# Kernel optimization log

Hardware: AMD Instinct MI355X
Metric: run time of the kernel (lower is better)

## Reference

```python
import jax, jax.numpy as jnp
import numpy as np

N = 50000
IN_DIM = 128
HID = 64
HEADS = 4
OUT_DIM = 2
NEG_SLOPE = 0.2


def setup_inputs() -> dict:
    key = jax.random.key(0)
    ks = jax.random.split(key, 10)
    x = jax.random.normal(ks[0], (N, IN_DIM), dtype=jnp.float32)
    edge_index = jax.random.randint(ks[1], (2, 800000), 0, N, dtype=jnp.int64)
    s = 0.1
    W1 = jax.random.normal(ks[2], (IN_DIM, HEADS * HID), dtype=jnp.float32) * s
    att_src1 = jax.random.normal(ks[3], (HEADS, HID), dtype=jnp.float32) * s
    att_dst1 = jax.random.normal(ks[4], (HEADS, HID), dtype=jnp.float32) * s
    b1 = jnp.zeros((HEADS * HID,), dtype=jnp.float32)
    W2 = jax.random.normal(ks[5], (HEADS * HID, 1 * OUT_DIM), dtype=jnp.float32) * s
    att_src2 = jax.random.normal(ks[6], (1, OUT_DIM), dtype=jnp.float32) * s
    att_dst2 = jax.random.normal(ks[7], (1, OUT_DIM), dtype=jnp.float32) * s
    b2 = jnp.zeros((OUT_DIM,), dtype=jnp.float32)
    return {"x": x, "edge_index": edge_index, "W1": W1, "att_src1": att_src1,
            "att_dst1": att_dst1, "b1": b1, "W2": W2, "att_src2": att_src2,
            "att_dst2": att_dst2, "b2": b2}


def gat_conv(x, W, att_src, att_dst, b, src, dst, heads, ch):
    # x: [N, F_in] -> h: [N, H, C]
    n = x.shape[0]
    h = (x @ W).reshape(n, heads, ch)
    a_s = jnp.einsum('nhc,hc->nh', h, att_src)  # [N, H]
    a_d = jnp.einsum('nhc,hc->nh', h, att_dst)  # [N, H]
    e = jax.nn.leaky_relu(a_s[src] + a_d[dst], NEG_SLOPE)  # [E, H]
    # segment softmax over incoming edges of each destination node
    m = jax.ops.segment_max(e, dst, num_segments=n)
    ex = jnp.exp(e - m[dst])
    z = jax.ops.segment_sum(ex, dst, num_segments=n)
    alpha = ex / z[dst]  # [E, H]
    msg = h[src] * alpha[:, :, None]  # [E, H, C]
    out = jax.ops.segment_sum(msg, dst, num_segments=n)  # [N, H, C]
    return out.reshape(n, heads * ch) + b


def reference(x, edge_index, W1, att_src1, att_dst1, b1, W2, att_src2, att_dst2, b2):
    n = x.shape[0]
    loop = jnp.arange(n, dtype=edge_index.dtype)
    src = jnp.concatenate([edge_index[0], loop])  # add_self_loops (PyG default)
    dst = jnp.concatenate([edge_index[1], loop])
    h = gat_conv(x, W1, att_src1, att_dst1, b1, src, dst, HEADS, HID)
    h = jax.nn.elu(h)
    # dropout is identity at inference
    out = gat_conv(h, W2, att_src2, att_dst2, b2, src, dst, 1, OUT_DIM)
    return out
```

## Files before the change

### kernel.cpp

```cpp
#include <hip/hip_runtime.h>

#define NN     50000
#define E_RAW  800000
#define ETOT   (E_RAW + NN)
#define FIN    128
#define FH     256
#define NEG    0.2f
#define BCAP   64

#define P_PART 8
#define DPW    6250
#define R_REP  32
#define EPW    (E_RAW / R_REP)
#define CNT_WGS (P_PART * R_REP)
#define PREP_WGS 8
#define SC2_NB  (P_PART * R_REP)
#define GEMM_NB ((NN + 63) / 64)

typedef __attribute__((ext_vector_type(8))) short s16x8;
typedef __attribute__((ext_vector_type(4))) float f32x4;

static __device__ __forceinline__ float leaky(float v) { return v > 0.f ? v : NEG * v; }

static __device__ __forceinline__ unsigned short f2bf(float f) {
    unsigned u = __float_as_uint(f);
    unsigned r = u + 0x7fffu + ((u >> 16) & 1u);
    return (unsigned short)(r >> 16);
}

__global__ __launch_bounds__(1024) void k_count(const int* __restrict__ ei,
                                                const float* __restrict__ W1,
                                                unsigned short* __restrict__ Wt_bf,
                                                int* __restrict__ pcnt)
{
    const int t = threadIdx.x;
    if (blockIdx.x >= CNT_WGS) {
        const int base = (blockIdx.x - CNT_WGS) * 4096;
        for (int i = t; i < 4096; i += 1024) {
            int idx = base + i;
            int k = idx >> 8, col = idx & 255;
            Wt_bf[col * FIN + k] = f2bf(W1[k * FH + col]);
        }
        return;
    }
    __shared__ int lcnt[DPW];
    const int p  = blockIdx.x >> 5;
    const int r  = blockIdx.x & 31;
    const int lo = p * DPW;
    for (int i = t; i < DPW; i += 1024) lcnt[i] = 0;
    __syncthreads();
    const int ebase = r * EPW, eend = ebase + EPW;
    for (int e0 = ebase + t * 4; e0 < eend; e0 += 4096) {
        int4 dv4 = *(const int4*)&ei[E_RAW + e0];
#pragma unroll
        for (int k = 0; k < 4; k++) {
            unsigned rel = (unsigned)((&dv4.x)[k] - lo);
            if (rel < DPW) atomicAdd(&lcnt[rel], 1);
        }
    }
    __syncthreads();
    for (int i = t; i < DPW; i += 1024)
        pcnt[r * NN + lo + i] = lcnt[i];
}

__global__ __launch_bounds__(1024) void k_gx(const float* __restrict__ x,
                                             const unsigned short* __restrict__ Wt_bf,
                                             const float* __restrict__ att_src,
                                             const float* __restrict__ att_dst,
                                             const int* __restrict__ ei,
                                             const int* __restrict__ pcnt,
                                             int* __restrict__ cnt,
                                             int* __restrict__ csr_src,
                                             unsigned short* __restrict__ h1b,
                                             float* __restrict__ a_s,
                                             float* __restrict__ a_d)
{
    __shared__ __align__(16) unsigned char SbufRaw[64 * 256 * 2];
    const int t = threadIdx.x;

    if (blockIdx.x < SC2_NB) {
        int* cur = (int*)SbufRaw;
        const int p  = blockIdx.x >> 5;
        const int r  = blockIdx.x & 31;
        const int lo = p * DPW;
        for (int i = t; i < DPW; i += 1024) {
            int d = lo + i;
            int run = 1;
            for (int rr = 0; rr < r; rr++)
                run += pcnt[rr * NN + d];
            cur[i] = run;
            if (r == R_REP - 1) cnt[d] = run + pcnt[r * NN + d];
            if (r == 0) csr_src[(size_t)d << 6] = d;
        }
        __syncthreads();
        const int ebase = r * EPW, eend = ebase + EPW;
        for (int e0 = ebase + t * 4; e0 < eend; e0 += 4096) {
            int4 sv4 = *(const int4*)&ei[e0];
            int4 dv4 = *(const int4*)&ei[E_RAW + e0];
#pragma unroll
            for (int k = 0; k < 4; k++) {
                int d = (&dv4.x)[k];
                unsigned rel = (unsigned)(d - lo);
                if (rel < DPW) {
                    int pos = atomicAdd(&cur[rel], 1);
                    if (pos < BCAP)
                        csr_src[((size_t)d << 6) + pos] = (&sv4.x)[k];
                }
            }
        }
        return;
    }

    if (t >= 256) return;
    unsigned short* Sbuf = (unsigned short*)SbufRaw;
    const int w    = t >> 6;
    const int lane = t & 63;
    const int li   = lane & 15;
    const int q8   = (lane >> 4) * 8;
    const int quad = lane >> 4;
    const int n0   = (blockIdx.x - SC2_NB) * 64;

    {
        const int node_l = t >> 2;
        const int k0 = (t & 3) * 32;
        int nn = n0 + node_l; if (nn >= NN) nn = NN - 1;
        const float* xp = &x[(size_t)nn * FIN + k0];
        unsigned short* xd = &Sbuf[node_l * 136 + k0];
#pragma unroll
        for (int i = 0; i < 8; i++) {
            float4 v = *(const float4*)&xp[i * 4];
            xd[i * 4 + 0] = f2bf(v.x);
            xd[i * 4 + 1] = f2bf(v.y);
            xd[i * 4 + 2] = f2bf(v.z);
            xd[i * 4 + 3] = f2bf(v.w);
        }
    }
    __syncthreads();

    f32x4 acc[4][4];
#pragma unroll
    for (int i = 0; i < 4; i++)
#pragma unroll
        for (int j = 0; j < 4; j++) acc[i][j] = (f32x4){0.f, 0.f, 0.f, 0.f};

#pragma unroll
    for (int kki = 0; kki < 4; kki++) {
        const int kk = kki * 32;
        s16x8 af[4], bf[4];
#pragma unroll
        for (int n16 = 0; n16 < 4; n16++) {
            int col = w * 64 + n16 * 16 + li;
            bf[n16] = *(const s16x8*)&Wt_bf[col * FIN + kk + q8];
        }
#pragma unroll
        for (int m16 = 0; m16 < 4; m16++)
            af[m16] = *(const s16x8*)&Sbuf[(m16 * 16 + li) * 136 + kk + q8];
#pragma unroll
        for (int m16 = 0; m16 < 4; m16++)
#pragma unroll
            for (int n16 = 0; n16 < 4; n16++)
                acc[m16][n16] = __builtin_amdgcn_mfma_f32_16x16x32_bf16(
                    af[m16], bf[n16], acc[m16][n16], 0, 0, 0);
    }

    {
        float as_c[4], ad_c[4];
#pragma unroll
        for (int n16 = 0; n16 < 4; n16++) {
            int col = w * 64 + n16 * 16 + li;
            as_c[n16] = att_src[col];
            ad_c[n16] = att_dst[col];
        }
#pragma unroll
        for (int m16 = 0; m16 < 4; m16++) {
            float ps[4], pd[4];
#pragma unroll
            for (int reg = 0; reg < 4; reg++) {
                float s = 0.f, d = 0.f;
#pragma unroll
                for (int n16 = 0; n16 < 4; n16++) {
                    s += acc[m16][n16][reg] * as_c[n16];
                    d += acc[m16][n16][reg] * ad_c[n16];
                }
                ps[reg] = s; pd[reg] = d;
            }
#pragma unroll
            for (int off = 1; off < 16; off <<= 1) {
#pragma unroll
                for (int reg = 0; reg < 4; reg++) {
                    ps[reg] += __shfl_xor(ps[reg], off);
                    pd[reg] += __shfl_xor(pd[reg], off);
                }
            }
            if (li == 0) {
#pragma unroll
                for (int reg = 0; reg < 4; reg++) {
                    int node = n0 + m16 * 16 + quad * 4 + reg;
                    if (node < NN) {
                        a_s[node * 4 + w] = ps[reg];
                        a_d[node * 4 + w] = pd[reg];
                    }
                }
            }
        }
    }

    __syncthreads();
#pragma unroll
    for (int m16 = 0; m16 < 4; m16++)
#pragma unroll
        for (int n16 = 0; n16 < 4; n16++)
#pragma unroll
            for (int reg = 0; reg < 4; reg++)
                Sbuf[(m16 * 16 + quad * 4 + reg) * FH + w * 64 + n16 * 16 + li] =
                    f2bf(acc[m16][n16][reg]);
    __syncthreads();
    {
        const int node_l = t >> 2;
        const int c0 = (t & 3) * 64;
        int node = n0 + node_l;
        if (node < NN) {
#pragma unroll
            for (int i = 0; i < 8; i++)
                *(uint4*)&h1b[(size_t)node * FH + c0 + i * 8] =
                    *(const uint4*)&Sbuf[node_l * FH + c0 + i * 8];
        }
    }
}

__global__ __launch_bounds__(256) void k_agg1(const int* __restrict__ cnt,
                                              const int* __restrict__ csr_src,
                                              const float* __restrict__ a_s1,
                                              const float* __restrict__ a_d1,
                                              const unsigned short* __restrict__ h1b,
                                              const float* __restrict__ b1,
                                              const float* __restrict__ W2,
                                              const float* __restrict__ att_src2,
                                              const float* __restrict__ att_dst2,
                                              float4* __restrict__ nd4)
{
    const int lane = threadIdx.x & 63;
    const int n = blockIdx.x * 4 + (threadIdx.x >> 6);
    if (n >= NN) return;
    int m = cnt[n]; if (m > BCAP) m = BCAP;
    const int h = lane >> 4;
    const float ad_h = a_d1[n * 4 + h];
    float acc0 = 0.f, acc1 = 0.f, acc2 = 0.f, acc3 = 0.f, z = 0.f;
    const int* sp = &csr_src[(size_t)n << 6];
#pragma unroll 4
    for (int j = 0; j < m; j++) {
        int s = sp[j];
        float as_h = a_s1[s * 4 + h];
        float ex = __expf(leaky(as_h + ad_h));
        unsigned long long wv =
            *(const unsigned long long*)(h1b + (size_t)s * FH + lane * 4);
        unsigned lo = (unsigned)wv, hi = (unsigned)(wv >> 32);
        acc0 += __uint_as_float(lo << 16) * ex;
        acc1 += __uint_as_float(lo & 0xffff0000u) * ex;
        acc2 += __uint_as_float(hi << 16) * ex;
        acc3 += __uint_as_float(hi & 0xffff0000u) * ex;
        z += ex;
    }
    const int c0 = lane * 4;
    float4 bb = *(const float4*)&b1[c0];
    float v0 = acc0 / z + bb.x;
    float v1 = acc1 / z + bb.y;
    float v2 = acc2 / z + bb.z;
    float v3 = acc3 / z + bb.w;
    v0 = v0 > 0.f ? v0 : __expf(v0) - 1.f;
    v1 = v1 > 0.f ? v1 : __expf(v1) - 1.f;
    v2 = v2 > 0.f ? v2 : __expf(v2) - 1.f;
    v3 = v3 > 0.f ? v3 : __expf(v3) - 1.f;
    float4 w2a = *(const float4*)&W2[c0 * 2];
    float4 w2b = *(const float4*)&W2[c0 * 2 + 4];
    float s0 = v0 * w2a.x + v1 * w2a.z + v2 * w2b.x + v3 * w2b.z;
    float s1 = v0 * w2a.y + v1 * w2a.w + v2 * w2b.y + v3 * w2b.w;
#pragma unroll
    for (int off = 32; off; off >>= 1) {
        s0 += __shfl_xor(s0, off);
        s1 += __shfl_xor(s1, off);
    }
    if (lane == 0) {
        float4 nd;
        nd.x = s0; nd.y = s1;
        nd.z = s0 * att_src2[0] + s1 * att_src2[1];
        nd.w = s0 * att_dst2[0] + s1 * att_dst2[1];
        nd4[n] = nd;
    }
}

__global__ __launch_bounds__(256) void k_agg2(const int* __restrict__ cnt,
                                              const int* __restrict__ csr_src,
                                              const float4* __restrict__ nd4,
                                              const float* __restrict__ b2,
                                              float* __restrict__ out)
{
    const int l = threadIdx.x & 15;
    const int n = blockIdx.x * 16 + (threadIdx.x >> 4);
    if (n >= NN) return;
    int m = cnt[n]; if (m > BCAP) m = BCAP;
    const int* sp = &csr_src[(size_t)n << 6];
    const float ad = nd4[n].w;
    float z = 0.f, a0 = 0.f, a1 = 0.f;
    for (int j = l; j < m; j += 16) {
        int s = sp[j];
        float4 f = nd4[s];
        float ex = __expf(leaky(f.z + ad));
        z  += ex;
        a0 += f.x * ex;
        a1 += f.y * ex;
    }
#pragma unroll
    for (int off = 8; off; off >>= 1) {
        z  += __shfl_xor(z, off);
        a0 += __shfl_xor(a0, off);
        a1 += __shfl_xor(a1, off);
    }
    if (l == 0) {
        out[n * 2 + 0] = a0 / z + b2[0];
        out[n * 2 + 1] = a1 / z + b2[1];
    }
}

extern "C" void kernel_launch(void* const* d_in, const int* in_sizes, int n_in,
                              void* d_out, int out_size, void* d_ws, size_t ws_size,
                              hipStream_t stream)
{
    const float* x        = (const float*)d_in[0];
    const int*   ei       = (const int*)d_in[1];
    const float* W1       = (const float*)d_in[2];
    const float* att_src1 = (const float*)d_in[3];
    const float* att_dst1 = (const float*)d_in[4];
    const float* b1       = (const float*)d_in[5];
    const float* W2       = (const float*)d_in[6];
    const float* att_src2 = (const float*)d_in[7];
    const float* att_dst2 = (const float*)d_in[8];
    const float* b2       = (const float*)d_in[9];
    float* out = (float*)d_out;

    int*    csr_src = (int*)d_ws;
    unsigned short* h1b = (unsigned short*)(csr_src + (size_t)NN * 64);
    unsigned short* Wt_bf = h1b + (size_t)NN * FH;
    int*    pcnt  = (int*)(Wt_bf + FH * FIN);
    int*    cnt   = pcnt + (size_t)NN * R_REP;
    float*  a_s1  = (float*)(cnt + NN);
    float*  a_d1  = a_s1 + (size_t)NN * 4;
    float4* nd4   = (float4*)(a_d1 + (size_t)NN * 4);

    k_count<<<CNT_WGS + PREP_WGS, 1024, 0, stream>>>(ei, W1, Wt_bf, pcnt);
    k_gx<<<SC2_NB + GEMM_NB, 1024, 0, stream>>>(x, Wt_bf, att_src1, att_dst1, ei,
                                                pcnt, cnt, csr_src, h1b, a_s1, a_d1);
    k_agg1<<<(NN + 3) / 4, 256, 0, stream>>>(cnt, csr_src, a_s1, a_d1, h1b,
                                             b1, W2, att_src2, att_dst2, nd4);
    k_agg2<<<(NN + 15) / 16, 256, 0, stream>>>(cnt, csr_src, nd4, b2, out);
}
```

Measured before the change: 228.3 us.

## Move GEMM into count kernel and split CSR scatter into its own launch

Restructures the front of the pipeline: a small prep kernel converts W1 to transposed bf16, then one 256-thread kernel runs both the per-partition degree counting and the layer-1 GEMM with attention logits, and a separate kernel does the CSR scatter. The GEMM no longer shares a launch with the scatter, where its 1024-thread blocks left 768 threads idle, and now overlaps with the counting pass instead. It adds an extra launch, and the front kernel still redundantly rewrites Wt_bf in its prep blocks while GEMM blocks read it, which is a benign race since the values are identical. Counting blocks drop to 256 threads, so each block processes its edge slice with fewer threads.

```diff
diff --git a/kernel.cpp b/kernel.cpp
--- a/kernel.cpp
+++ b/kernel.cpp
@@ -13,8 +13,7 @@
 #define R_REP  32
 #define EPW    (E_RAW / R_REP)
 #define CNT_WGS (P_PART * R_REP)
-#define PREP_WGS 8
-#define SC2_NB  (P_PART * R_REP)
+#define PREP_NB 8
 #define GEMM_NB ((NN + 63) / 64)
 
 typedef __attribute__((ext_vector_type(8))) short s16x8;
@@ -28,97 +27,60 @@
     return (unsigned short)(r >> 16);
 }
 
-__global__ __launch_bounds__(1024) void k_count(const int* __restrict__ ei,
-                                                const float* __restrict__ W1,
-                                                unsigned short* __restrict__ Wt_bf,
-                                                int* __restrict__ pcnt)
-{
+__global__ __launch_bounds__(256) void k_front(const int* __restrict__ ei,
+                                               const float* __restrict__ W1,
+                                               const float* __restrict__ x,
+                                               const unsigned short* __restrict__ Wt_bf_c,
+                                               unsigned short* __restrict__ Wt_bf,
+                                               int* __restrict__ pcnt,
+                                               const float* __restrict__ att_src,
+                                               const float* __restrict__ att_dst,
+                                               unsigned short* __restrict__ h1b,
+                                               float* __restrict__ a_s,
+                                               float* __restrict__ a_d)
+{
+    __shared__ __align__(16) unsigned char SbufRaw[64 * 256 * 2];
     const int t = threadIdx.x;
-    if (blockIdx.x >= CNT_WGS) {
+
+    if (blockIdx.x < CNT_WGS) {
+        int* lcnt = (int*)SbufRaw;
+        const int p  = blockIdx.x >> 5;
+        const int r  = blockIdx.x & 31;
+        const int lo = p * DPW;
+        for (int i = t; i < DPW; i += 256) lcnt[i] = 0;
+        __syncthreads();
+        const int ebase = r * EPW, eend = ebase + EPW;
+        for (int e0 = ebase + t * 4; e0 < eend; e0 += 1024) {
+            int4 dv4 = *(const int4*)&ei[E_RAW + e0];
+#pragma unroll
+            for (int k = 0; k < 4; k++) {
+                unsigned rel = (unsigned)((&dv4.x)[k] - lo);
+                if (rel < DPW) atomicAdd(&lcnt[rel], 1);
+            }
+        }
+        __syncthreads();
+        for (int i = t; i < DPW; i += 256)
+            pcnt[r * NN + lo + i] = lcnt[i];
+        return;
+    }
+
+    if (blockIdx.x < CNT_WGS + PREP_NB) {
         const int base = (blockIdx.x - CNT_WGS) * 4096;
-        for (int i = t; i < 4096; i += 1024) {
+        for (int i = t; i < 4096; i += 256) {
             int idx = base + i;
             int k = idx >> 8, col = idx & 255;
             Wt_bf[col * FIN + k] = f2bf(W1[k * FH + col]);
         }
         return;
     }
-    __shared__ int lcnt[DPW];
-    const int p  = blockIdx.x >> 5;
-    const int r  = blockIdx.x & 31;
-    const int lo = p * DPW;
-    for (int i = t; i < DPW; i += 1024) lcnt[i] = 0;
-    __syncthreads();
-    const int ebase = r * EPW, eend = ebase + EPW;
-    for (int e0 = ebase + t * 4; e0 < eend; e0 += 4096) {
-        int4 dv4 = *(const int4*)&ei[E_RAW + e0];
-#pragma unroll
-        for (int k = 0; k < 4; k++) {
-            unsigned rel = (unsigned)((&dv4.x)[k] - lo);
-            if (rel < DPW) atomicAdd(&lcnt[rel], 1);
-        }
-    }
-    __syncthreads();
-    for (int i = t; i < DPW; i += 1024)
-        pcnt[r * NN + lo + i] = lcnt[i];
-}
-
-__global__ __launch_bounds__(1024) void k_gx(const float* __restrict__ x,
-                                             const unsigned short* __restrict__ Wt_bf,
-                                             const float* __restrict__ att_src,
-                                             const float* __restrict__ att_dst,
-                                             const int* __restrict__ ei,
-                                             const int* __restrict__ pcnt,
-                                             int* __restrict__ cnt,
-                                             int* __restrict__ csr_src,
-                                             unsigned short* __restrict__ h1b,
-                                             float* __restrict__ a_s,
-                                             float* __restrict__ a_d)
-{
-    __shared__ __align__(16) unsigned char SbufRaw[64 * 256 * 2];
-    const int t = threadIdx.x;
-
-    if (blockIdx.x < SC2_NB) {
-        int* cur = (int*)SbufRaw;
-        const int p  = blockIdx.x >> 5;
-        const int r  = blockIdx.x & 31;
-        const int lo = p * DPW;
-        for (int i = t; i < DPW; i += 1024) {
-            int d = lo + i;
-            int run = 1;
-            for (int rr = 0; rr < r; rr++)
-                run += pcnt[rr * NN + d];
-            cur[i] = run;
-            if (r == R_REP - 1) cnt[d] = run + pcnt[r * NN + d];
-            if (r == 0) csr_src[(size_t)d << 6] = d;
-        }
-        __syncthreads();
-        const int ebase = r * EPW, eend = ebase + EPW;
-        for (int e0 = ebase + t * 4; e0 < eend; e0 += 4096) {
-            int4 sv4 = *(const int4*)&ei[e0];
-            int4 dv4 = *(const int4*)&ei[E_RAW + e0];
-#pragma unroll
-            for (int k = 0; k < 4; k++) {
-                int d = (&dv4.x)[k];
-                unsigned rel = (unsigned)(d - lo);
-                if (rel < DPW) {
-                    int pos = atomicAdd(&cur[rel], 1);
-                    if (pos < BCAP)
-                        csr_src[((size_t)d << 6) + pos] = (&sv4.x)[k];
-                }
-            }
-        }
-        return;
-    }
-
-    if (t >= 256) return;
+
     unsigned short* Sbuf = (unsigned short*)SbufRaw;
     const int w    = t >> 6;
     const int lane = t & 63;
     const int li   = lane & 15;
     const int q8   = (lane >> 4) * 8;
     const int quad = lane >> 4;
-    const int n0   = (blockIdx.x - SC2_NB) * 64;
+    const int n0   = (blockIdx.x - CNT_WGS - PREP_NB) * 64;
 
     {
         const int node_l = t >> 2;
@@ -150,7 +112,7 @@
 #pragma unroll
         for (int n16 = 0; n16 < 4; n16++) {
             int col = w * 64 + n16 * 16 + li;
-            bf[n16] = *(const s16x8*)&Wt_bf[col * FIN + kk + q8];
+            bf[n16] = *(const s16x8*)&Wt_bf_c[col * FIN + kk + q8];
         }
 #pragma unroll
         for (int m16 = 0; m16 < 4; m16++)
@@ -224,6 +186,43 @@
             for (int i = 0; i < 8; i++)
                 *(uint4*)&h1b[(size_t)node * FH + c0 + i * 8] =
                     *(const uint4*)&Sbuf[node_l * FH + c0 + i * 8];
+        }
+    }
+}
+
+__global__ __launch_bounds__(1024) void k_scat(const int* __restrict__ ei,
+                                               const int* __restrict__ pcnt,
+                                               int* __restrict__ cnt,
+                                               int* __restrict__ csr_src)
+{
+    __shared__ int cur[DPW];
+    const int t  = threadIdx.x;
+    const int p  = blockIdx.x >> 5;
+    const int r  = blockIdx.x & 31;
+    const int lo = p * DPW;
+    for (int i = t; i < DPW; i += 1024) {
+        int d = lo + i;
+        int run = 1;
+        for (int rr = 0; rr < r; rr++)
+            run += pcnt[rr * NN + d];
+        cur[i] = run;
+        if (r == R_REP - 1) cnt[d] = run + pcnt[r * NN + d];
+        if (r == 0) csr_src[(size_t)d << 6] = d;
+    }
+    __syncthreads();
+    const int ebase = r * EPW, eend = ebase + EPW;
+    for (int e0 = ebase + t * 4; e0 < eend; e0 += 4096) {
+        int4 sv4 = *(const int4*)&ei[e0];
+        int4 dv4 = *(const int4*)&ei[E_RAW + e0];
+#pragma unroll
+        for (int k = 0; k < 4; k++) {
+            int d = (&dv4.x)[k];
+            unsigned rel = (unsigned)(d - lo);
+            if (rel < DPW) {
+                int pos = atomicAdd(&cur[rel], 1);
+                if (pos < BCAP)
+                    csr_src[((size_t)d << 6) + pos] = (&sv4.x)[k];
+            }
         }
     }
 }
@@ -347,9 +346,24 @@
     float*  a_d1  = a_s1 + (size_t)NN * 4;
     float4* nd4   = (float4*)(a_d1 + (size_t)NN * 4);
 
-    k_count<<<CNT_WGS + PREP_WGS, 1024, 0, stream>>>(ei, W1, Wt_bf, pcnt);
-    k_gx<<<SC2_NB + GEMM_NB, 1024, 0, stream>>>(x, Wt_bf, att_src1, att_dst1, ei,
-                                                pcnt, cnt, csr_src, h1b, a_s1, a_d1);
+    {
+        struct Launcher {
+            static __global__ __launch_bounds__(256) void prep(
+                const float* __restrict__ W1, unsigned short* __restrict__ Wt_bf)
+            {
+                const int base = blockIdx.x * 4096;
+                for (int i = threadIdx.x; i < 4096; i += 256) {
+                    int idx = base + i;
+                    int k = idx >> 8, col = idx & 255;
+                    Wt_bf[col * FIN + k] = f2bf(W1[k * FH + col]);
+                }
+            }
+        };
+        Launcher::prep<<<PREP_NB, 256, 0, stream>>>(W1, Wt_bf);
+    }
+    k_front<<<CNT_WGS + PREP_NB + GEMM_NB, 256, 0, stream>>>(
+        ei, W1, x, Wt_bf, Wt_bf, pcnt, att_src1, att_dst1, h1b, a_s1, a_d1);
+    k_scat<<<CNT_WGS, 1024, 0, stream>>>(ei, pcnt, cnt, csr_src);
     k_agg1<<<(NN + 3) / 4, 256, 0, stream>>>(cnt, csr_src, a_s1, a_d1, h1b,
                                              b1, W2, att_src2, att_dst2, nd4);
     k_agg2<<<(NN + 15) / 16, 256, 0, stream>>>(cnt, csr_src, nd4, b2, out);
```

After: 231.7 us. Within noise of the previous version (+1.5%).
